# Performance work log

Hardware: AMD Instinct MI355X
Metric: run time of the kernel (lower is better)

## Reference

```python
import jax, jax.numpy as jnp
import numpy as np

N, E, F_IN, NUM_GRAPHS, K = 50000, 500000, 160, 128, 3


def _glorot(k, shape):
    lim = np.sqrt(6.0 / (shape[-2] + shape[-1])).astype(np.float32)
    return jax.random.uniform(k, shape, jnp.float32, -lim, lim)


def setup_inputs() -> dict:
    key = jax.random.key(0)
    ks = jax.random.split(key, 8)
    x = jax.random.normal(ks[0], (N, F_IN), jnp.float32)
    edge_index = jax.random.randint(ks[1], (2, E), 0, N)
    edge_attr = jax.random.uniform(ks[2], (E,), jnp.float32)
    batch = jnp.sort(jax.random.randint(ks[3], (N,), 0, NUM_GRAPHS))
    W1 = _glorot(ks[4], (K, F_IN, 128)); b1 = jnp.zeros((128,), jnp.float32)
    W2 = _glorot(ks[5], (K, 128, 64)); b2 = jnp.zeros((64,), jnp.float32)
    W3 = _glorot(ks[6], (K, 64, 32)); b3 = jnp.zeros((32,), jnp.float32)
    Wl = _glorot(ks[7], (32, 2)); bl = jnp.zeros((2,), jnp.float32)
    return dict(x=x, edge_index=edge_index, edge_attr=edge_attr, batch=batch,
                W1=W1, b1=b1, W2=W2, b2=b2, W3=W3, b3=b3, Wl=Wl, bl=bl)


def _cheb_norm(src, dst, edge_attr, n):
    # PyG ChebConv: sym-normalized Laplacian, lambda_max=2 =>
    # L_hat = (2/lmax)*L_sym - I = -D^{-1/2} A D^{-1/2} (diagonal = 0)
    deg = jax.ops.segment_sum(edge_attr, src, num_segments=n)
    safe = jnp.where(deg > 0, deg, 1.0)
    dinv = jnp.where(deg > 0, jax.lax.rsqrt(safe), 0.0)
    return -dinv[src] * edge_attr * dinv[dst]


def _propagate(x, src, dst, w, n):
    # out[dst] += w * x[src]  (sparse L_hat @ x)
    return jax.ops.segment_sum(w[:, None] * x[src], dst, num_segments=n)


def _cheb_conv(x, src, dst, w, W, b, n):
    # Chebyshev recurrence: T0 = x, T1 = L_hat x, Tk = 2 L_hat T(k-1) - T(k-2)
    tx0 = x
    out = tx0 @ W[0]
    tx1 = _propagate(tx0, src, dst, w, n)
    out = out + tx1 @ W[1]
    for k in range(2, W.shape[0]):
        tx2 = 2.0 * _propagate(tx1, src, dst, w, n) - tx0
        out = out + tx2 @ W[k]
        tx0, tx1 = tx1, tx2
    return out + b


def reference(x, edge_index, edge_attr, batch, W1, b1, W2, b2, W3, b3, Wl, bl):
    n = x.shape[0]
    src, dst = edge_index[0], edge_index[1]
    w = _cheb_norm(src, dst, edge_attr, n)
    h = jax.nn.relu(_cheb_conv(x, src, dst, w, W1, b1, n))
    h = jax.nn.relu(_cheb_conv(h, src, dst, w, W2, b2, n))
    h = jax.nn.relu(_cheb_conv(h, src, dst, w, W3, b3, n))
    # global_mean_pool over graph ids (dropout omitted: eval mode)
    sums = jax.ops.segment_sum(h, batch, num_segments=NUM_GRAPHS)
    cnt = jax.ops.segment_sum(jnp.ones((n,), h.dtype), batch, num_segments=NUM_GRAPHS)
    pooled = sums / jnp.maximum(cnt, 1.0)[:, None]
    return pooled @ Wl + bl
```

## Files before the change

### kernel.cpp

```cpp
#include <hip/hip_runtime.h>

#define N_NODES 50000
#define N_EDGES 500000
#define NUM_G   128
#define SCAN_NB 49
#define PN      (SCAN_NB * 1024)
#define NCX     64
#define ECH     7813
#define RNG     8192
#define NRY     7
#define HVB     (2 * NCX * NRY)
#define CONVB   7813
#define WPREPB  360
#define SCVB    (NCX * NRY)
#define GEMM_MB 782

typedef __attribute__((ext_vector_type(8))) short short8;
typedef __attribute__((ext_vector_type(4))) float f32x4;

__device__ __forceinline__ unsigned f2bf(float x) {
    unsigned u = __float_as_uint(x);
    return (u + 0x7FFFu + ((u >> 16) & 1u)) >> 16;
}
__device__ __forceinline__ float bf2f(unsigned h) {
    return __uint_as_float(h << 16);
}

__device__ __forceinline__ void wprep_one(const float* __restrict__ W, unsigned short* __restrict__ WT,
                                          int t, int FIN, int F) {
    int n = t / FIN, k = t - n * FIN;
    int sel = n / F, c = n - sel * F;
    float v;
    if (sel == 0) v = W[(size_t)k * F + c] - W[(size_t)2 * FIN * F + (size_t)k * F + c];
    else          v = W[(size_t)sel * FIN * F + (size_t)k * F + c];
    WT[t] = (unsigned short)f2bf(v);
}

__global__ __launch_bounds__(256)
void prep_kernel(const int* __restrict__ src, const int* __restrict__ dst,
                 const float* __restrict__ ea,
                 float* __restrict__ pdeg, int* __restrict__ pcnt,
                 const float* __restrict__ x, unsigned short* __restrict__ Xb,
                 const float* __restrict__ W1, const float* __restrict__ W2,
                 const float* __restrict__ W3,
                 unsigned short* __restrict__ WT1, unsigned short* __restrict__ WT2,
                 unsigned short* __restrict__ WT3) {
    __shared__ unsigned lh[RNG];
    int vb = blockIdx.x, tid = threadIdx.x;
    if (vb < HVB) {
        bool isdeg = vb < NCX * NRY;
        int v2 = isdeg ? vb : vb - NCX * NRY;
        int xk = v2 & 63, y = v2 >> 6;
        int base = y * RNG;
        for (int i = tid; i < RNG; i += 256) lh[i] = 0u;
        __syncthreads();
        int e0 = xk * ECH, e1 = min(e0 + ECH, N_EDGES);
        if (isdeg) {
            for (int e = e0 + tid; e < e1; e += 256) {
                int s = src[e];
                if ((unsigned)(s - base) < RNG) atomicAdd((float*)&lh[s - base], ea[e]);
            }
        } else {
            for (int e = e0 + tid; e < e1; e += 256) {
                int d = dst[e];
                if ((unsigned)(d - base) < RNG) atomicAdd((int*)&lh[d - base], 1);
            }
        }
        __syncthreads();
        if (isdeg) {
            for (int i = tid; i < RNG; i += 256) {
                int n = base + i;
                if (n < PN) pdeg[(size_t)xk * PN + n] = ((float*)lh)[i];
            }
        } else {
            for (int i = tid; i < RNG; i += 256) {
                int n = base + i;
                if (n < PN) pcnt[(size_t)xk * PN + n] = ((int*)lh)[i];
            }
        }
    } else if (vb < HVB + CONVB) {
        int t = (vb - HVB) * 256 + tid;
        if (t < N_NODES * 160 / 4) {
            float4 v = reinterpret_cast<const float4*>(x)[t];
            ushort4 r;
            r.x = (unsigned short)f2bf(v.x);
            r.y = (unsigned short)f2bf(v.y);
            r.z = (unsigned short)f2bf(v.z);
            r.w = (unsigned short)f2bf(v.w);
            *reinterpret_cast<ushort4*>(Xb + (size_t)t * 4) = r;
        }
    } else {
        int t = (vb - HVB - CONVB) * 256 + tid;
        if (t < 61440)      wprep_one(W1, WT1, t, 160, 128);
        else if (t < 86016) wprep_one(W2, WT2, t - 61440, 128, 64);
        else if (t < 92160) wprep_one(W3, WT3, t - 86016, 64, 32);
    }
}

__global__ __launch_bounds__(256)
void reduce_scan_kernel(const float* __restrict__ pdeg, int* __restrict__ pcnt,
                        float* __restrict__ dinv, int* __restrict__ cnt,
                        int* __restrict__ partial) {
    int b = blockIdx.x, t = threadIdx.x;
    int i0 = b * 1024 + t * 4;
    float d0 = 0.f, d1 = 0.f, d2 = 0.f, d3 = 0.f;
    int r0 = 0, r1 = 0, r2 = 0, r3 = 0;
    for (int x = 0; x < NCX; ++x) {
        float4 pv = *reinterpret_cast<const float4*>(pdeg + (size_t)x * PN + i0);
        int4   cv = *reinterpret_cast<const int4*>(pcnt + (size_t)x * PN + i0);
        *reinterpret_cast<int4*>(pcnt + (size_t)x * PN + i0) = make_int4(r0, r1, r2, r3);
        d0 += pv.x; d1 += pv.y; d2 += pv.z; d3 += pv.w;
        r0 += cv.x; r1 += cv.y; r2 += cv.z; r3 += cv.w;
    }
    float dd[4] = {d0, d1, d2, d3};
    int   rr[4] = {r0, r1, r2, r3};
    int s = 0;
    #pragma unroll
    for (int j = 0; j < 4; ++j) {
        int n = i0 + j;
        if (n < N_NODES) {
            float dv = dd[j], r = 0.f;
            if (dv > 0.f) {
                r = rsqrtf(dv);
                r = r * (1.5f - 0.5f * dv * r * r);
            }
            dinv[n] = r;
            cnt[n] = rr[j];
            s += rr[j];
        } else {
            cnt[n] = 0;
        }
    }
    __shared__ int red[256];
    red[t] = s;
    __syncthreads();
    for (int off = 128; off > 0; off >>= 1) {
        if (t < off) red[t] += red[t + off];
        __syncthreads();
    }
    if (t == 0) partial[b] = red[0];
}

__global__ __launch_bounds__(256)
void scan_final_kernel(const int* __restrict__ cnt, const int* __restrict__ partial,
                       int* __restrict__ rowptr, int n) {
    int b = blockIdx.x, t = threadIdx.x;
    __shared__ int red[256];
    __shared__ int sh_off, sh_tot;
    if (t < 64) {
        int orig = (t < SCAN_NB) ? partial[t] : 0;
        int v = orig;
        #pragma unroll
        for (int off = 1; off < 64; off <<= 1) {
            int u = __shfl_up(v, off, 64);
            if (t >= off) v += u;
        }
        if (t == b) sh_off = v - orig;
        if (t == SCAN_NB - 1) sh_tot = v;
    }
    __syncthreads();
    int4 v = reinterpret_cast<const int4*>(cnt)[b * 256 + t];
    int s = v.x + v.y + v.z + v.w;
    red[t] = s;
    __syncthreads();
    for (int off = 1; off < 256; off <<= 1) {
        int u = (t >= off) ? red[t - off] : 0;
        __syncthreads();
        red[t] += u;
        __syncthreads();
    }
    int excl = sh_off + ((t == 0) ? 0 : red[t - 1]);
    int i0 = b * 1024 + t * 4;
    if (i0 < n)     rowptr[i0]     = excl;
    if (i0 + 1 < n) rowptr[i0 + 1] = excl + v.x;
    if (i0 + 2 < n) rowptr[i0 + 2] = excl + v.x + v.y;
    if (i0 + 3 < n) rowptr[i0 + 3] = excl + v.x + v.y + v.z;
    if (b == SCAN_NB - 1 && t == 0) rowptr[n] = sh_tot;
}

__device__ void scatter_body(int vb, const int* __restrict__ src, const int* __restrict__ dst,
                             const float* __restrict__ ea,
                             const int* __restrict__ rowptr, const int* __restrict__ pcnt,
                             int2* __restrict__ csr, unsigned char* smraw) {
    int* cursor = (int*)smraw;
    int tid = threadIdx.x;
    int x = vb & 63, y = vb >> 6;
    int base = y * RNG;
    for (int i = tid; i < RNG; i += 256) {
        int n = base + i;
        cursor[i] = (n < N_NODES) ? (rowptr[n] + pcnt[(size_t)x * PN + n]) : 0;
    }
    __syncthreads();
    int e0 = x * ECH, e1 = min(e0 + ECH, N_EDGES);
    for (int e = e0 + tid; e < e1; e += 256) {
        int d = dst[e];
        if ((unsigned)(d - base) < RNG) {
            int pos = atomicAdd(&cursor[d - base], 1);
            int2 ew;
            ew.x = src[e];
            ew.y = __float_as_int(ea[e]);
            csr[pos] = ew;
        }
    }
}

template<int FIN, int F>
__device__ void gemm_body(int bx, int g, const unsigned short* __restrict__ Xb,
                          const unsigned short* __restrict__ WT, const float* __restrict__ dinv,
                          unsigned short* __restrict__ Y0, unsigned short* __restrict__ Y1,
                          unsigned short* __restrict__ Y2, int nrows, unsigned char* smraw) {
    constexpr int KT = FIN / 32;
    constexpr int NT = F / 32;
    constexpr int SA = FIN + 8;
    constexpr int F8 = FIN / 8;
    short* Bs = (short*)smraw;

    int tid = threadIdx.x;
    int lane = tid & 63, w = tid >> 6;
    int m0 = bx * 64;
    unsigned short* Ys = (g == 0) ? Y0 : (g == 1) ? Y1 : Y2;

    int colb = lane & 15;
    int q8 = (lane >> 4) << 3;
    int rq = (lane >> 4) << 2;
    int arow = m0 + w * 16 + colb;
    bool rok = arow < nrows;

    short8 afr[KT];
    #pragma unroll
    for (int kt = 0; kt < KT; ++kt) {
        short8 z = {0, 0, 0, 0, 0, 0, 0, 0};
        afr[kt] = rok ? *reinterpret_cast<const short8*>(Xb + (size_t)arow * FIN + (kt << 5) + q8) : z;
    }

    for (int nt = 0; nt < NT; ++nt) {
        int n0 = (g * NT + nt) << 5;
        __syncthreads();
        for (int span = tid; span < 32 * F8; span += 256) {
            int r = span / F8, c8 = (span - r * F8) << 3;
            int pr = (r < 16) ? (r << 1) : (((r - 16) << 1) + 1);
            *reinterpret_cast<uint4*>(&Bs[r * SA + c8]) =
                *reinterpret_cast<const uint4*>(WT + (size_t)(n0 + pr) * FIN + c8);
        }
        __syncthreads();

        f32x4 acc0 = {0.f, 0.f, 0.f, 0.f}, acc1 = acc0;
        #pragma unroll
        for (int kt = 0; kt < KT; ++kt) {
            short8 b0 = *reinterpret_cast<const short8*>(&Bs[colb * SA + (kt << 5) + q8]);
            short8 b1 = *reinterpret_cast<const short8*>(&Bs[(colb + 16) * SA + (kt << 5) + q8]);
            acc0 = __builtin_amdgcn_mfma_f32_16x16x32_bf16(afr[kt], b0, acc0, 0, 0, 0);
            acc1 = __builtin_amdgcn_mfma_f32_16x16x32_bf16(afr[kt], b1, acc1, 0, 0, 0);
        }

        int lc = (nt << 5) + (colb << 1);
        #pragma unroll
        for (int r = 0; r < 4; ++r) {
            int orow = m0 + w * 16 + rq + r;
            if (orow < nrows) {
                float sc = (g == 2) ? dinv[orow] : 1.0f;
                unsigned pack = f2bf(acc0[r] * sc) | (f2bf(acc1[r] * sc) << 16);
                *reinterpret_cast<unsigned*>(Ys + (size_t)orow * F + lc) = pack;
            }
        }
    }
}

__global__ __launch_bounds__(256)
void sg_kernel(const int* __restrict__ src, const int* __restrict__ dst,
               const float* __restrict__ ea,
               const int* __restrict__ rowptr, const int* __restrict__ pcnt,
               int2* __restrict__ csr,
               const unsigned short* __restrict__ Xb, const unsigned short* __restrict__ WT1,
               const float* __restrict__ dinv,
               unsigned short* __restrict__ Y0, unsigned short* __restrict__ Y1,
               unsigned short* __restrict__ Y2) {
    __shared__ alignas(16) unsigned char sm[32768];
    int vb = blockIdx.x;
    if (vb < SCVB) {
        scatter_body(vb, src, dst, ea, rowptr, pcnt, csr, sm);
    } else {
        int v2 = vb - SCVB;
        gemm_body<160, 128>(v2 % GEMM_MB, v2 / GEMM_MB, Xb, WT1, dinv, Y0, Y1, Y2, N_NODES, sm);
    }
}

template<int FIN, int F>
__launch_bounds__(256)
__global__ void cheb_gemm(const unsigned short* __restrict__ Xb, const unsigned short* __restrict__ WT,
                          const float* __restrict__ dinv,
                          unsigned short* __restrict__ Y0, unsigned short* __restrict__ Y1,
                          unsigned short* __restrict__ Y2, int nrows) {
    __shared__ alignas(16) unsigned char sm[32 * (FIN + 8) * 2];
    gemm_body<FIN, F>(blockIdx.x, blockIdx.y, Xb, WT, dinv, Y0, Y1, Y2, nrows, sm);
}

__device__ __forceinline__ void acc8(float* acc, uint4 p, float wv) {
    acc[0] += wv * bf2f(p.x & 0xFFFFu);
    acc[1] += wv * __uint_as_float(p.x & 0xFFFF0000u);
    acc[2] += wv * bf2f(p.y & 0xFFFFu);
    acc[3] += wv * __uint_as_float(p.y & 0xFFFF0000u);
    acc[4] += wv * bf2f(p.z & 0xFFFFu);
    acc[5] += wv * __uint_as_float(p.z & 0xFFFF0000u);
    acc[6] += wv * bf2f(p.w & 0xFFFFu);
    acc[7] += wv * __uint_as_float(p.w & 0xFFFF0000u);
}

__device__ __forceinline__ void expand8(uint4 p, float* o) {
    o[0] = bf2f(p.x & 0xFFFFu);
    o[1] = __uint_as_float(p.x & 0xFFFF0000u);
    o[2] = bf2f(p.y & 0xFFFFu);
    o[3] = __uint_as_float(p.y & 0xFFFF0000u);
    o[4] = bf2f(p.z & 0xFFFFu);
    o[5] = __uint_as_float(p.z & 0xFFFF0000u);
    o[6] = bf2f(p.w & 0xFFFFu);
    o[7] = __uint_as_float(p.w & 0xFFFF0000u);
}

template<int F, int MODE>
__launch_bounds__(256)
__global__ void gather_kernel(const unsigned short* __restrict__ X, const int2* __restrict__ csr,
                              const int* __restrict__ rowptr, const float* __restrict__ dinv,
                              const unsigned short* __restrict__ Y, const float* __restrict__ bias,
                              unsigned short* __restrict__ O, int n) {
    constexpr int FQ8 = F >> 3;
    constexpr int DPB = 256 / FQ8;
    constexpr int CAP = 2048;
    __shared__ int2 scsr[CAP];
    __shared__ int srp[DPB + 1];
    int tid = threadIdx.x;
    int db0 = blockIdx.x * DPB;
    if (tid <= DPB) srp[tid] = rowptr[min(db0 + tid, n)];
    __syncthreads();
    int ebeg = srp[0];
    int ecnt = srp[DPB] - ebeg;
    bool staged = ecnt <= CAP;
    if (staged) {
        for (int i = tid; i < ecnt; i += 256)
            scsr[i] = csr[ebeg + i];
    }
    __syncthreads();

    int d = db0 + tid / FQ8;
    if (d >= n) return;
    int f8 = (tid % FQ8) << 3;
    float acc[8] = {0.f, 0.f, 0.f, 0.f, 0.f, 0.f, 0.f, 0.f};

    if (staged) {
        int beg = srp[tid / FQ8] - ebeg, end = srp[tid / FQ8 + 1] - ebeg;
        int i = beg;
        for (; i + 7 < end; i += 8) {
            int2 e0 = scsr[i],     e1 = scsr[i + 1], e2 = scsr[i + 2], e3 = scsr[i + 3];
            int2 e4 = scsr[i + 4], e5 = scsr[i + 5], e6 = scsr[i + 6], e7 = scsr[i + 7];
            uint4 p0 = *reinterpret_cast<const uint4*>(X + (size_t)e0.x * F + f8);
            uint4 p1 = *reinterpret_cast<const uint4*>(X + (size_t)e1.x * F + f8);
            uint4 p2 = *reinterpret_cast<const uint4*>(X + (size_t)e2.x * F + f8);
            uint4 p3 = *reinterpret_cast<const uint4*>(X + (size_t)e3.x * F + f8);
            uint4 p4 = *reinterpret_cast<const uint4*>(X + (size_t)e4.x * F + f8);
            uint4 p5 = *reinterpret_cast<const uint4*>(X + (size_t)e5.x * F + f8);
            uint4 p6 = *reinterpret_cast<const uint4*>(X + (size_t)e6.x * F + f8);
            uint4 p7 = *reinterpret_cast<const uint4*>(X + (size_t)e7.x * F + f8);
            acc8(acc, p0, __int_as_float(e0.y));
            acc8(acc, p1, __int_as_float(e1.y));
            acc8(acc, p2, __int_as_float(e2.y));
            acc8(acc, p3, __int_as_float(e3.y));
            acc8(acc, p4, __int_as_float(e4.y));
            acc8(acc, p5, __int_as_float(e5.y));
            acc8(acc, p6, __int_as_float(e6.y));
            acc8(acc, p7, __int_as_float(e7.y));
        }
        for (; i + 3 < end; i += 4) {
            int2 e0 = scsr[i], e1 = scsr[i + 1], e2 = scsr[i + 2], e3 = scsr[i + 3];
            uint4 p0 = *reinterpret_cast<const uint4*>(X + (size_t)e0.x * F + f8);
            uint4 p1 = *reinterpret_cast<const uint4*>(X + (size_t)e1.x * F + f8);
            uint4 p2 = *reinterpret_cast<const uint4*>(X + (size_t)e2.x * F + f8);
            uint4 p3 = *reinterpret_cast<const uint4*>(X + (size_t)e3.x * F + f8);
            acc8(acc, p0, __int_as_float(e0.y));
            acc8(acc, p1, __int_as_float(e1.y));
            acc8(acc, p2, __int_as_float(e2.y));
            acc8(acc, p3, __int_as_float(e3.y));
        }
        for (; i < end; ++i) {
            int2 e = scsr[i];
            uint4 p = *reinterpret_cast<const uint4*>(X + (size_t)e.x * F + f8);
            acc8(acc, p, __int_as_float(e.y));
        }
    } else {
        int beg = srp[tid / FQ8], end = srp[tid / FQ8 + 1];
        for (int i = beg; i < end; ++i) {
            int2 e = csr[i];
            uint4 p = *reinterpret_cast<const uint4*>(X + (size_t)e.x * F + f8);
            acc8(acc, p, __int_as_float(e.y));
        }
    }

    float y[8];
    expand8(*reinterpret_cast<const uint4*>(Y + (size_t)d * F + f8), y);
    float dv = dinv[d];
    float v[8];
    if (MODE == 0) {
        float dv2 = 2.f * dv;
        #pragma unroll
        for (int j = 0; j < 8; ++j) v[j] = dv * (y[j] - dv2 * acc[j]);
    } else {
        float4 ba = *reinterpret_cast<const float4*>(bias + f8);
        float4 bb = *reinterpret_cast<const float4*>(bias + f8 + 4);
        v[0] = fmaxf(y[0] - dv * acc[0] + ba.x, 0.f);
        v[1] = fmaxf(y[1] - dv * acc[1] + ba.y, 0.f);
        v[2] = fmaxf(y[2] - dv * acc[2] + ba.z, 0.f);
        v[3] = fmaxf(y[3] - dv * acc[3] + ba.w, 0.f);
        v[4] = fmaxf(y[4] - dv * acc[4] + bb.x, 0.f);
        v[5] = fmaxf(y[5] - dv * acc[5] + bb.y, 0.f);
        v[6] = fmaxf(y[6] - dv * acc[6] + bb.z, 0.f);
        v[7] = fmaxf(y[7] - dv * acc[7] + bb.w, 0.f);
    }
    uint4 o;
    o.x = f2bf(v[0]) | (f2bf(v[1]) << 16);
    o.y = f2bf(v[2]) | (f2bf(v[3]) << 16);
    o.z = f2bf(v[4]) | (f2bf(v[5]) << 16);
    o.w = f2bf(v[6]) | (f2bf(v[7]) << 16);
    *reinterpret_cast<uint4*>(O + (size_t)d * F + f8) = o;
}

__device__ __forceinline__ int lower_bound_dev(const int* __restrict__ a, int n, int v) {
    int lo = 0, hi = n;
    while (lo < hi) {
        int mid = (lo + hi) >> 1;
        if (a[mid] < v) lo = mid + 1; else hi = mid;
    }
    return lo;
}

__global__ void pool_kernel(const unsigned short* __restrict__ H, const int* __restrict__ batch,
                            const float* __restrict__ Wl, const float* __restrict__ bl,
                            float* __restrict__ out, int n) {
    int g = blockIdx.x;
    int start = lower_bound_dev(batch, n, g);
    int end   = lower_bound_dev(batch, n, g + 1);
    int tid = threadIdx.x;
    int f = tid & 31;
    int sub = tid >> 5;
    float acc = 0.0f;
    for (int i = start + sub; i < end; i += 8)
        acc += bf2f((unsigned)H[(size_t)i * 32 + f]);
    __shared__ float red[256];
    red[tid] = acc;
    __syncthreads();
    if (tid < 128) red[tid] += red[tid + 128];
    __syncthreads();
    if (tid < 64) red[tid] += red[tid + 64];
    __syncthreads();
    if (tid < 32) red[tid] += red[tid + 32];
    __syncthreads();
    if (tid < 2) {
        int cnt = end - start;
        float inv = 1.0f / (float)(cnt > 0 ? cnt : 1);
        float o = bl[tid];
        for (int f2 = 0; f2 < 32; ++f2)
            o += red[f2] * inv * Wl[f2 * 2 + tid];
        out[g * 2 + tid] = o;
    }
}

extern "C" void kernel_launch(void* const* d_in, const int* in_sizes, int n_in,
                              void* d_out, int out_size, void* d_ws, size_t ws_size,
                              hipStream_t stream) {
    const float* x     = (const float*)d_in[0];
    const int*   ei    = (const int*)d_in[1];
    const float* ea    = (const float*)d_in[2];
    const int*   batch = (const int*)d_in[3];
    const float* W1 = (const float*)d_in[4];
    const float* b1 = (const float*)d_in[5];
    const float* W2 = (const float*)d_in[6];
    const float* b2 = (const float*)d_in[7];
    const float* W3 = (const float*)d_in[8];
    const float* b3 = (const float*)d_in[9];
    const float* Wl = (const float*)d_in[10];
    const float* bl = (const float*)d_in[11];
    float* out = (float*)d_out;
    char* ws = (char*)d_ws;

    const int* src = ei;
    const int* dst = ei + N_EDGES;

    size_t off = 0;
    auto alloc = [&](size_t bytes) { char* p = ws + off; off += (bytes + 255) & ~(size_t)255; return p; };
    float* pdeg    = (float*)alloc((size_t)NCX * PN * 4);
    int*   pcnt    = (int*)  alloc((size_t)NCX * PN * 4);
    float* dinv    = (float*)alloc(N_NODES * 4);
    int*   cnt     = (int*)  alloc((size_t)PN * 4);
    int*   partial = (int*)  alloc(SCAN_NB * 4);
    int*   rowptr  = (int*)  alloc((N_NODES + 1) * 4);
    int2*  csr     = (int2*) alloc((size_t)N_EDGES * 8);
    unsigned short* Xb  = (unsigned short*)alloc((size_t)N_NODES * 160 * 2);
    unsigned short* Y0  = (unsigned short*)alloc((size_t)N_NODES * 128 * 2);
    unsigned short* Y1  = (unsigned short*)alloc((size_t)N_NODES * 128 * 2);
    unsigned short* Y2  = (unsigned short*)alloc((size_t)N_NODES * 128 * 2);
    unsigned short* U   = (unsigned short*)alloc((size_t)N_NODES * 128 * 2);
    unsigned short* WT1 = (unsigned short*)alloc((size_t)384 * 160 * 2);
    unsigned short* WT2 = (unsigned short*)alloc((size_t)192 * 128 * 2);
    unsigned short* WT3 = (unsigned short*)alloc((size_t)96 * 64 * 2);

    const int BT = 256;

    prep_kernel<<<HVB + CONVB + WPREPB, BT, 0, stream>>>(src, dst, ea, pdeg, pcnt,
                                                         x, Xb, W1, W2, W3, WT1, WT2, WT3);
    reduce_scan_kernel<<<SCAN_NB, BT, 0, stream>>>(pdeg, pcnt, dinv, cnt, partial);
    scan_final_kernel<<<SCAN_NB, BT, 0, stream>>>(cnt, partial, rowptr, N_NODES);
    sg_kernel<<<SCVB + 3 * GEMM_MB, BT, 0, stream>>>(src, dst, ea, rowptr, pcnt, csr,
                                                     Xb, WT1, dinv, Y0, Y1, Y2);

    dim3 ggrid(GEMM_MB, 3);
    auto gb = [&](int F) { int DPB = 256 / (F / 8); return (N_NODES + DPB - 1) / DPB; };

    gather_kernel<128, 0><<<gb(128), BT, 0, stream>>>(Y2, csr, rowptr, dinv, Y1, nullptr, U, N_NODES);
    gather_kernel<128, 1><<<gb(128), BT, 0, stream>>>(U, csr, rowptr, dinv, Y0, b1, Xb, N_NODES);

    cheb_gemm<128, 64><<<ggrid, BT, 0, stream>>>(Xb, WT2, dinv, Y0, Y1, Y2, N_NODES);
    gather_kernel<64, 0><<<gb(64), BT, 0, stream>>>(Y2, csr, rowptr, dinv, Y1, nullptr, U, N_NODES);
    gather_kernel<64, 1><<<gb(64), BT, 0, stream>>>(U, csr, rowptr, dinv, Y0, b2, Xb, N_NODES);

    cheb_gemm<64, 32><<<ggrid, BT, 0, stream>>>(Xb, WT3, dinv, Y0, Y1, Y2, N_NODES);
    gather_kernel<32, 0><<<gb(32), BT, 0, stream>>>(Y2, csr, rowptr, dinv, Y1, nullptr, U, N_NODES);
    gather_kernel<32, 1><<<gb(32), BT, 0, stream>>>(U, csr, rowptr, dinv, Y0, b3, Xb, N_NODES);

    pool_kernel<<<NUM_G, BT, 0, stream>>>(Xb, batch, Wl, bl, out, N_NODES);
}
```

Baseline: 312.0 us.

## Merge degree and count histograms into one pass; move conversions into reduce kernel

Degree and in-count histograms are now built by one kernel that reads src, dst and edge_attr once per edge, with two 32 KB LDS arrays, instead of separate blocks each rescanning the edges. The x-to-bf16 conversion and weight prep blocks move from the histogram launch into the reduce/scan launch, so they overlap with the small reduction work rather than the histogram. This cuts redundant edge reads, at the cost of doubled LDS per block, which lowers occupancy, and fewer histogram blocks (448 versus 896).

```diff
diff --git a/kernel.cpp b/kernel.cpp
--- a/kernel.cpp
+++ b/kernel.cpp
@@ -9,7 +9,6 @@
 #define ECH     7813
 #define RNG     8192
 #define NRY     7
-#define HVB     (2 * NCX * NRY)
 #define CONVB   7813
 #define WPREPB  360
 #define SCVB    (NCX * NRY)
@@ -24,6 +23,33 @@
 }
 __device__ __forceinline__ float bf2f(unsigned h) {
     return __uint_as_float(h << 16);
+}
+
+__global__ __launch_bounds__(256)
+void hist_kernel(const int* __restrict__ src, const int* __restrict__ dst,
+                 const float* __restrict__ ea,
+                 float* __restrict__ pdeg, int* __restrict__ pcnt) {
+    __shared__ float ldeg[RNG];
+    __shared__ int   lcnt[RNG];
+    int xk = blockIdx.x, y = blockIdx.y, tid = threadIdx.x;
+    int base = y * RNG;
+    for (int i = tid; i < RNG; i += 256) { ldeg[i] = 0.f; lcnt[i] = 0; }
+    __syncthreads();
+    int e0 = xk * ECH, e1 = min(e0 + ECH, N_EDGES);
+    for (int e = e0 + tid; e < e1; e += 256) {
+        int s = src[e], d = dst[e];
+        float a = ea[e];
+        if ((unsigned)(s - base) < RNG) atomicAdd(&ldeg[s - base], a);
+        if ((unsigned)(d - base) < RNG) atomicAdd(&lcnt[d - base], 1);
+    }
+    __syncthreads();
+    for (int i = tid; i < RNG; i += 256) {
+        int n = base + i;
+        if (n < PN) {
+            pdeg[(size_t)xk * PN + n] = ldeg[i];
+            pcnt[(size_t)xk * PN + n] = lcnt[i];
+        }
+    }
 }
 
 __device__ __forceinline__ void wprep_one(const float* __restrict__ W, unsigned short* __restrict__ WT,
@@ -37,108 +63,70 @@
 }
 
 __global__ __launch_bounds__(256)
-void prep_kernel(const int* __restrict__ src, const int* __restrict__ dst,
-                 const float* __restrict__ ea,
-                 float* __restrict__ pdeg, int* __restrict__ pcnt,
-                 const float* __restrict__ x, unsigned short* __restrict__ Xb,
-                 const float* __restrict__ W1, const float* __restrict__ W2,
-                 const float* __restrict__ W3,
-                 unsigned short* __restrict__ WT1, unsigned short* __restrict__ WT2,
-                 unsigned short* __restrict__ WT3) {
-    __shared__ unsigned lh[RNG];
-    int vb = blockIdx.x, tid = threadIdx.x;
-    if (vb < HVB) {
-        bool isdeg = vb < NCX * NRY;
-        int v2 = isdeg ? vb : vb - NCX * NRY;
-        int xk = v2 & 63, y = v2 >> 6;
-        int base = y * RNG;
-        for (int i = tid; i < RNG; i += 256) lh[i] = 0u;
+void rs_kernel(const float* __restrict__ pdeg, int* __restrict__ pcnt,
+               float* __restrict__ dinv, int* __restrict__ cnt, int* __restrict__ partial,
+               const float* __restrict__ x, unsigned short* __restrict__ Xb,
+               const float* __restrict__ W1, const float* __restrict__ W2,
+               const float* __restrict__ W3,
+               unsigned short* __restrict__ WT1, unsigned short* __restrict__ WT2,
+               unsigned short* __restrict__ WT3) {
+    __shared__ int red[256];
+    int vb = blockIdx.x, t = threadIdx.x;
+    if (vb < SCAN_NB) {
+        int b = vb;
+        int i0 = b * 1024 + t * 4;
+        float d0 = 0.f, d1 = 0.f, d2 = 0.f, d3 = 0.f;
+        int r0 = 0, r1 = 0, r2 = 0, r3 = 0;
+        for (int xk = 0; xk < NCX; ++xk) {
+            float4 pv = *reinterpret_cast<const float4*>(pdeg + (size_t)xk * PN + i0);
+            int4   cv = *reinterpret_cast<const int4*>(pcnt + (size_t)xk * PN + i0);
+            *reinterpret_cast<int4*>(pcnt + (size_t)xk * PN + i0) = make_int4(r0, r1, r2, r3);
+            d0 += pv.x; d1 += pv.y; d2 += pv.z; d3 += pv.w;
+            r0 += cv.x; r1 += cv.y; r2 += cv.z; r3 += cv.w;
+        }
+        float dd[4] = {d0, d1, d2, d3};
+        int   rr[4] = {r0, r1, r2, r3};
+        int s = 0;
+        #pragma unroll
+        for (int j = 0; j < 4; ++j) {
+            int n = i0 + j;
+            if (n < N_NODES) {
+                float dv = dd[j], r = 0.f;
+                if (dv > 0.f) {
+                    r = rsqrtf(dv);
+                    r = r * (1.5f - 0.5f * dv * r * r);
+                }
+                dinv[n] = r;
+                cnt[n] = rr[j];
+                s += rr[j];
+            } else {
+                cnt[n] = 0;
+            }
+        }
+        red[t] = s;
         __syncthreads();
-        int e0 = xk * ECH, e1 = min(e0 + ECH, N_EDGES);
-        if (isdeg) {
-            for (int e = e0 + tid; e < e1; e += 256) {
-                int s = src[e];
-                if ((unsigned)(s - base) < RNG) atomicAdd((float*)&lh[s - base], ea[e]);
-            }
-        } else {
-            for (int e = e0 + tid; e < e1; e += 256) {
-                int d = dst[e];
-                if ((unsigned)(d - base) < RNG) atomicAdd((int*)&lh[d - base], 1);
-            }
-        }
-        __syncthreads();
-        if (isdeg) {
-            for (int i = tid; i < RNG; i += 256) {
-                int n = base + i;
-                if (n < PN) pdeg[(size_t)xk * PN + n] = ((float*)lh)[i];
-            }
-        } else {
-            for (int i = tid; i < RNG; i += 256) {
-                int n = base + i;
-                if (n < PN) pcnt[(size_t)xk * PN + n] = ((int*)lh)[i];
-            }
-        }
-    } else if (vb < HVB + CONVB) {
-        int t = (vb - HVB) * 256 + tid;
-        if (t < N_NODES * 160 / 4) {
-            float4 v = reinterpret_cast<const float4*>(x)[t];
+        for (int off = 128; off > 0; off >>= 1) {
+            if (t < off) red[t] += red[t + off];
+            __syncthreads();
+        }
+        if (t == 0) partial[b] = red[0];
+    } else if (vb < SCAN_NB + CONVB) {
+        int tt = (vb - SCAN_NB) * 256 + t;
+        if (tt < N_NODES * 160 / 4) {
+            float4 v = reinterpret_cast<const float4*>(x)[tt];
             ushort4 r;
             r.x = (unsigned short)f2bf(v.x);
             r.y = (unsigned short)f2bf(v.y);
             r.z = (unsigned short)f2bf(v.z);
             r.w = (unsigned short)f2bf(v.w);
-            *reinterpret_cast<ushort4*>(Xb + (size_t)t * 4) = r;
+            *reinterpret_cast<ushort4*>(Xb + (size_t)tt * 4) = r;
         }
     } else {
-        int t = (vb - HVB - CONVB) * 256 + tid;
-        if (t < 61440)      wprep_one(W1, WT1, t, 160, 128);
-        else if (t < 86016) wprep_one(W2, WT2, t - 61440, 128, 64);
-        else if (t < 92160) wprep_one(W3, WT3, t - 86016, 64, 32);
-    }
-}
-
-__global__ __launch_bounds__(256)
-void reduce_scan_kernel(const float* __restrict__ pdeg, int* __restrict__ pcnt,
-                        float* __restrict__ dinv, int* __restrict__ cnt,
-                        int* __restrict__ partial) {
-    int b = blockIdx.x, t = threadIdx.x;
-    int i0 = b * 1024 + t * 4;
-    float d0 = 0.f, d1 = 0.f, d2 = 0.f, d3 = 0.f;
-    int r0 = 0, r1 = 0, r2 = 0, r3 = 0;
-    for (int x = 0; x < NCX; ++x) {
-        float4 pv = *reinterpret_cast<const float4*>(pdeg + (size_t)x * PN + i0);
-        int4   cv = *reinterpret_cast<const int4*>(pcnt + (size_t)x * PN + i0);
-        *reinterpret_cast<int4*>(pcnt + (size_t)x * PN + i0) = make_int4(r0, r1, r2, r3);
-        d0 += pv.x; d1 += pv.y; d2 += pv.z; d3 += pv.w;
-        r0 += cv.x; r1 += cv.y; r2 += cv.z; r3 += cv.w;
-    }
-    float dd[4] = {d0, d1, d2, d3};
-    int   rr[4] = {r0, r1, r2, r3};
-    int s = 0;
-    #pragma unroll
-    for (int j = 0; j < 4; ++j) {
-        int n = i0 + j;
-        if (n < N_NODES) {
-            float dv = dd[j], r = 0.f;
-            if (dv > 0.f) {
-                r = rsqrtf(dv);
-                r = r * (1.5f - 0.5f * dv * r * r);
-            }
-            dinv[n] = r;
-            cnt[n] = rr[j];
-            s += rr[j];
-        } else {
-            cnt[n] = 0;
-        }
-    }
-    __shared__ int red[256];
-    red[t] = s;
-    __syncthreads();
-    for (int off = 128; off > 0; off >>= 1) {
-        if (t < off) red[t] += red[t + off];
-        __syncthreads();
-    }
-    if (t == 0) partial[b] = red[0];
+        int tt = (vb - SCAN_NB - CONVB) * 256 + t;
+        if (tt < 61440)      wprep_one(W1, WT1, tt, 160, 128);
+        else if (tt < 86016) wprep_one(W2, WT2, tt - 61440, 128, 64);
+        else if (tt < 92160) wprep_one(W3, WT3, tt - 86016, 64, 32);
+    }
 }
 
 __global__ __launch_bounds__(256)
@@ -503,9 +491,9 @@
 
     const int BT = 256;
 
-    prep_kernel<<<HVB + CONVB + WPREPB, BT, 0, stream>>>(src, dst, ea, pdeg, pcnt,
-                                                         x, Xb, W1, W2, W3, WT1, WT2, WT3);
-    reduce_scan_kernel<<<SCAN_NB, BT, 0, stream>>>(pdeg, pcnt, dinv, cnt, partial);
+    hist_kernel<<<dim3(NCX, NRY), BT, 0, stream>>>(src, dst, ea, pdeg, pcnt);
+    rs_kernel<<<SCAN_NB + CONVB + WPREPB, BT, 0, stream>>>(pdeg, pcnt, dinv, cnt, partial,
+                                                           x, Xb, W1, W2, W3, WT1, WT2, WT3);
     scan_final_kernel<<<SCAN_NB, BT, 0, stream>>>(cnt, partial, rowptr, N_NODES);
     sg_kernel<<<SCVB + 3 * GEMM_MB, BT, 0, stream>>>(src, dst, ea, rowptr, pcnt, csr,
                                                      Xb, WT1, dinv, Y0, Y1, Y2);
```

Measured after the change: 316.2 us. Within noise of the previous version (+1.3%).
